# Kernel tuning notes

Measured on AMD Instinct MI355X. Metric: run time of the kernel, lower is better.

Reference implementation:

```python
import jax, jax.numpy as jnp
import numpy as np

MIN_NORM = 1e-15
PROJ_EPS = 4e-3  # float32 boundary eps used by hgcn PoincareBall.proj
C = 1.0          # curvature for every layer
N, E, D = 10000, 320000, 256


def _norm(x):
    return jnp.maximum(jnp.linalg.norm(x, axis=-1, keepdims=True), MIN_NORM)


def artanh(x):
    return jnp.arctanh(jnp.clip(x, -1 + 1e-7, 1 - 1e-7))


def proj(x, c):
    norm = _norm(x)
    maxnorm = (1.0 - PROJ_EPS) / jnp.sqrt(c)
    return jnp.where(norm > maxnorm, x / norm * maxnorm, x)


def expmap0(u, c):
    sqrt_c = jnp.sqrt(c)
    u_norm = _norm(u)
    return jnp.tanh(sqrt_c * u_norm) * u / (sqrt_c * u_norm)


def logmap0(p, c):
    sqrt_c = jnp.sqrt(c)
    p_norm = _norm(p)
    return artanh(sqrt_c * p_norm) * p / (sqrt_c * p_norm)


def mobius_add(x, y, c):
    x2 = jnp.sum(x * x, -1, keepdims=True)
    y2 = jnp.sum(y * y, -1, keepdims=True)
    xy = jnp.sum(x * y, -1, keepdims=True)
    num = (1 + 2 * c * xy + c * y2) * x + (1 - c * x2) * y
    denom = 1 + 2 * c * xy + c * c * x2 * y2
    return num / jnp.maximum(denom, MIN_NORM)


def mobius_matvec(m, x, c):
    sqrt_c = jnp.sqrt(c)
    x_norm = _norm(x)
    mx = x @ m.T
    mx_norm = _norm(mx)
    res = jnp.tanh(mx_norm / x_norm * artanh(sqrt_c * x_norm)) * mx / (mx_norm * sqrt_c)
    zero_row = jnp.all(mx == 0, axis=-1, keepdims=True)
    return jnp.where(zero_row, jnp.zeros_like(res), res)


def hgc_layer(h, W, b, edge_weight, edge_src, edge_dst, c):
    # HypLinear (dropout=0, eval mode)
    res = proj(mobius_matvec(W, h, c), c)
    hyp_bias = proj(expmap0(b[None, :], c), c)
    h = proj(mobius_add(res, hyp_bias, c), c)
    # HypAgg: tangent-space neighborhood aggregation (spmm over edge list)
    xt = logmap0(h, c)                                  # [N, D]
    msgs = edge_weight[:, None] * xt[edge_src]          # [E, D] irregular gather
    agg = jax.ops.segment_sum(msgs, edge_dst, num_segments=N)
    h = proj(expmap0(agg, c), c)
    # HypAct: relu in tangent space, map back with c_out
    xt = jax.nn.relu(logmap0(h, c))
    return proj(expmap0(xt, c), c)


def setup_inputs() -> dict:
    key = jax.random.key(0)
    ks = jax.random.split(key, 8)
    x = jax.random.normal(ks[0], (N, D), dtype=jnp.float32)
    edge_src = jax.random.randint(ks[1], (E,), 0, N)
    edge_dst = jax.random.randint(ks[2], (E,), 0, N)
    # normalized-adjacency-like positive weights (~1/deg scale)
    edge_weight = jax.random.uniform(ks[3], (E,), dtype=jnp.float32) / 32.0
    s = 1.0 / np.sqrt(D)
    W1 = jax.random.normal(ks[4], (D, D), dtype=jnp.float32) * s
    b1 = jnp.zeros((D,), dtype=jnp.float32)
    W2 = jax.random.normal(ks[5], (D, D), dtype=jnp.float32) * s
    b2 = jnp.zeros((D,), dtype=jnp.float32)
    return {"x": x, "W1": W1, "b1": b1, "W2": W2, "b2": b2,
            "edge_weight": edge_weight, "edge_src": edge_src, "edge_dst": edge_dst}


def reference(x, W1, b1, W2, b2, edge_weight, edge_src, edge_dst):
    # old=True path: map Euclidean features onto the Poincare ball first
    h = proj(expmap0(x, C), C)
    h = hgc_layer(h, W1, b1, edge_weight, edge_src, edge_dst, C)
    h = hgc_layer(h, W2, b2, edge_weight, edge_src, edge_dst, C)
    return h
```

## Files before the change

### kernel.cpp

```cpp
#include <hip/hip_runtime.h>
#include <hip/hip_fp16.h>

#define DIM 256
#define MAXNORM 0.996f
#define MINN 1e-15f
#define CLIPV 0.9999999f
#define CAP 128

typedef __attribute__((ext_vector_type(8))) short bf16x8;
typedef __attribute__((ext_vector_type(4))) float f32x4;

__device__ __forceinline__ unsigned short f2bf(float f) {
    unsigned int u = __float_as_uint(f);
    u += 0x7fffu + ((u >> 16) & 1u);
    return (unsigned short)(u >> 16);
}
__device__ __forceinline__ float h2f(unsigned short h) {
    return __half2float(__ushort_as_half(h));
}
__device__ __forceinline__ unsigned short f2h(float f) {
    return __half_as_ushort(__float2half(f));
}
__device__ __forceinline__ float wsum(float v) {
    v += __shfl_xor(v, 32);
    v += __shfl_xor(v, 16);
    v += __shfl_xor(v, 8);
    v += __shfl_xor(v, 4);
    v += __shfl_xor(v, 2);
    v += __shfl_xor(v, 1);
    return v;
}
__device__ __forceinline__ float gsum16(float v) {
    v += __shfl_xor(v, 8);
    v += __shfl_xor(v, 4);
    v += __shfl_xor(v, 2);
    v += __shfl_xor(v, 1);
    return v;
}

__global__ void k_setup(const float* __restrict__ x, unsigned short* __restrict__ h_bf,
                        float* __restrict__ hnorm2, int nrows,
                        int* __restrict__ cnt,
                        const float* __restrict__ W1, const float* __restrict__ W2,
                        unsigned short* __restrict__ w_bf, int nPerW, int eB) {
    int bid = blockIdx.x;
    if (bid < eB) {
        int gid = bid * 256 + threadIdx.x;
        int row = gid >> 6, lane = gid & 63;
        if (row >= nrows) return;
        size_t base = (size_t)row * DIM + lane * 4;
        float4 v = *(const float4*)(x + base);
        float ss = wsum(v.x * v.x + v.y * v.y + v.z * v.z + v.w * v.w);
        float n = fmaxf(sqrtf(ss), MINN);
        float tn = tanhf(n);
        float hn = (tn > MAXNORM) ? MAXNORM : tn;
        float s = hn / n;
        ushort4 ob;
        ob.x = f2bf(v.x * s); ob.y = f2bf(v.y * s);
        ob.z = f2bf(v.z * s); ob.w = f2bf(v.w * s);
        *(ushort4*)(h_bf + base) = ob;
        if (lane == 0) hnorm2[row] = hn * hn;
    } else if (bid < eB + 8) {
        int i = (bid - eB) * 256 + threadIdx.x;
        int stride = 8 * 256;
        for (; i < nrows; i += stride) cnt[i] = 0;
    } else {
        int i = (bid - eB - 8) * 256 + threadIdx.x;
        int stride = 128 * 256;
        for (; i < 2 * nPerW; i += stride)
            w_bf[i] = f2bf(i < nPerW ? W1[i] : W2[i - nPerW]);
    }
}

__global__ void k_fill(const int* __restrict__ esrc, const int* __restrict__ edst,
                       const float* __restrict__ ew, int* __restrict__ cnt,
                       int2* __restrict__ bucket, int nE, int nrows) {
    int e = blockIdx.x * blockDim.x + threadIdx.x;
    if (e >= nE) return;
    int d = edst[e];
    if (d < 0 || d >= nrows) return;
    int pos = atomicAdd(&cnt[d], 1);
    if (pos < CAP)
        bucket[(size_t)d * CAP + pos] = make_int2(esrc[e], __float_as_int(ew[e]));
}

__global__ void k_gemm_post(const unsigned short* __restrict__ Abf,
                            const unsigned short* __restrict__ Wbf,
                            const float* __restrict__ hnorm2,
                            const float* __restrict__ bias,
                            unsigned short* __restrict__ XT, int M) {
    int wave = threadIdx.x >> 6;
    int lane = threadIdx.x & 63;
    int r = lane & 15, oct = lane >> 4;
    int i0 = (blockIdx.x * 4 + wave) * 16;
    int arow = i0 + r;
    bool av = arow < M;
    const unsigned short* ap = Abf + (size_t)(av ? arow : 0) * DIM + oct * 8;
    const unsigned short* wp = Wbf + (size_t)r * DIM + oct * 8;
    const bf16x8 zf = {0, 0, 0, 0, 0, 0, 0, 0};
    f32x4 acc[16];
#pragma unroll
    for (int jt = 0; jt < 16; ++jt) acc[jt] = (f32x4){0.f, 0.f, 0.f, 0.f};
    for (int k0 = 0; k0 < 256; k0 += 32) {
        bf16x8 a = av ? *(const bf16x8*)(ap + k0) : zf;
#pragma unroll
        for (int jt = 0; jt < 16; ++jt) {
            bf16x8 w = *(const bf16x8*)(wp + (size_t)jt * 16 * DIM + k0);
            acc[jt] = __builtin_amdgcn_mfma_f32_16x16x32_bf16(a, w, acc[jt], 0, 0, 0);
        }
    }
    float bv[16];
    float bss = 0.f;
#pragma unroll
    for (int jt = 0; jt < 16; ++jt) {
        bv[jt] = bias[jt * 16 + r];
        bss = fmaf(bv[jt], bv[jt], bss);
    }
    bss = gsum16(bss);
    float bn = fmaxf(sqrtf(bss), MINN);
    float btn = tanhf(bn);
    float bhn = (btn > MAXNORM) ? MAXNORM : btn;
    float bscale = bhn / bn;
    float y2 = bhn * bhn;
#pragma unroll
    for (int jt = 0; jt < 16; ++jt) bv[jt] *= bscale;

#pragma unroll
    for (int q = 0; q < 4; ++q) {
        int row = i0 + oct * 4 + q;
        float sm = 0.f, sxy = 0.f;
#pragma unroll
        for (int jt = 0; jt < 16; ++jt) {
            float m = acc[jt][q];
            sm  = fmaf(m, m, sm);
            sxy = fmaf(m, bv[jt], sxy);
        }
        sm = gsum16(sm);
        sxy = gsum16(sxy);
        if (row < M) {
            float sh = hnorm2[row];
            float xn = fmaxf(sqrtf(sh), MINN);
            float at = atanhf(fminf(xn, CLIPV));
            float mn = fmaxf(sqrtf(sm), MINN);
            float t = tanhf(mn / xn * at);
            float alpha = t / mn;
            float resn = t;
            if (t > MAXNORM) { alpha = MAXNORM / mn; resn = MAXNORM; }
            float x2 = resn * resn;
            float xy = alpha * sxy;
            float Aa = 1.f + 2.f * xy + y2;
            float Bb = 1.f - x2;
            float den = fmaxf(1.f + 2.f * xy + x2 * y2, MINN);
            float s_m = Aa * alpha / den;
            float s_b = Bb / den;
            float hn2 = (Aa * Aa * x2 + 2.f * Aa * Bb * xy + Bb * Bb * y2) / (den * den);
            float hn = fmaxf(sqrtf(fmaxf(hn2, 0.f)), MINN);
            if (hn > MAXNORM) { float f = MAXNORM / hn; s_m *= f; s_b *= f; hn = MAXNORM; }
            float lt = atanhf(fminf(hn, CLIPV)) / hn;
            s_m *= lt; s_b *= lt;
#pragma unroll
            for (int jt = 0; jt < 16; ++jt)
                XT[(size_t)row * DIM + jt * 16 + r] = f2h(fmaf(s_m, acc[jt][q], s_b * bv[jt]));
        }
    }
}

__global__ void k_agg_finish(const unsigned short* __restrict__ XT, const int* __restrict__ cnt,
                             const int2* __restrict__ bucket,
                             float* __restrict__ OUT, unsigned short* __restrict__ OUT_bf,
                             float* __restrict__ hnorm2, int nrows) {
    int gid = blockIdx.x * blockDim.x + threadIdx.x;
    int row = gid >> 6, lane = gid & 63;
    if (row >= nrows) return;
    int deg = cnt[row];
    if (deg > CAP) deg = CAP;
    const int2* cpk = bucket + (size_t)row * CAP;
    int p1 = deg;
    float a0 = 0.f, a1 = 0.f, a2 = 0.f, a3 = 0.f;
    int p = 0;
    for (; p + 7 < p1; p += 8) {
        ushort4 v[8];
        float w[8];
#pragma unroll
        for (int u = 0; u < 8; ++u) {
            int2 pk = cpk[p + u];
            w[u] = __int_as_float(pk.y);
            v[u] = *(const ushort4*)(XT + (size_t)pk.x * DIM + lane * 4);
        }
#pragma unroll
        for (int u = 0; u < 8; ++u) {
            a0 = fmaf(w[u], h2f(v[u].x), a0);
            a1 = fmaf(w[u], h2f(v[u].y), a1);
            a2 = fmaf(w[u], h2f(v[u].z), a2);
            a3 = fmaf(w[u], h2f(v[u].w), a3);
        }
    }
    for (; p < p1; ++p) {
        int2 pk = cpk[p];
        float w = __int_as_float(pk.y);
        ushort4 v = *(const ushort4*)(XT + (size_t)pk.x * DIM + lane * 4);
        a0 = fmaf(w, h2f(v.x), a0); a1 = fmaf(w, h2f(v.y), a1);
        a2 = fmaf(w, h2f(v.z), a2); a3 = fmaf(w, h2f(v.w), a3);
    }
    float ss = wsum(a0 * a0 + a1 * a1 + a2 * a2 + a3 * a3);
    float n = fmaxf(sqrtf(ss), MINN);
    float tn = tanhf(n);
    float hn = (tn > MAXNORM) ? MAXNORM : tn;
    float s1 = hn / n;
    float lt = atanhf(fminf(hn, CLIPV)) / fmaxf(hn, MINN);
    float s2 = lt * s1;
    float x0 = fmaxf(s2 * a0, 0.f), x1 = fmaxf(s2 * a1, 0.f);
    float x2 = fmaxf(s2 * a2, 0.f), x3 = fmaxf(s2 * a3, 0.f);
    float ss2 = wsum(x0 * x0 + x1 * x1 + x2 * x2 + x3 * x3);
    float n2 = fmaxf(sqrtf(ss2), MINN);
    float tn2 = tanhf(n2);
    float hn2c = (tn2 > MAXNORM) ? MAXNORM : tn2;
    float s3 = hn2c / n2;
    float o0 = s3 * x0, o1 = s3 * x1, o2 = s3 * x2, o3 = s3 * x3;
    size_t base = (size_t)row * DIM + lane * 4;
    if (OUT_bf) {
        ushort4 ob;
        ob.x = f2bf(o0); ob.y = f2bf(o1); ob.z = f2bf(o2); ob.w = f2bf(o3);
        *(ushort4*)(OUT_bf + base) = ob;
        if (lane == 0) hnorm2[row] = hn2c * hn2c;
    } else {
        *(float4*)(OUT + base) = make_float4(o0, o1, o2, o3);
    }
}

static inline size_t align256(size_t x) { return (x + 255) & ~(size_t)255; }

extern "C" void kernel_launch(void* const* d_in, const int* in_sizes, int n_in,
                              void* d_out, int out_size, void* d_ws, size_t ws_size,
                              hipStream_t stream) {
    const float* x  = (const float*)d_in[0];
    const float* W1 = (const float*)d_in[1];
    const float* b1 = (const float*)d_in[2];
    const float* W2 = (const float*)d_in[3];
    const float* b2 = (const float*)d_in[4];
    const float* ew = (const float*)d_in[5];
    const int* esrc = (const int*)d_in[6];
    const int* edst = (const int*)d_in[7];
    const int nE = in_sizes[5];
    const int M  = in_sizes[0] / DIM;

    size_t S = (size_t)M * DIM;
    char* base = (char*)d_ws;
    size_t o = 0;
    int2* bucket   = (int2*)(base + o);          o = align256(o + (size_t)M * CAP * 8);
    int* cnt       = (int*)(base + o);           o = align256(o + (size_t)M * 4);
    float* hnorm2  = (float*)(base + o);         o = align256(o + (size_t)(M + 64) * 4);
    unsigned short* xt   = (unsigned short*)(base + o);  o = align256(o + S * 2);
    unsigned short* h_bf = (unsigned short*)(base + o);  o = align256(o + S * 2);
    unsigned short* w_bf = (unsigned short*)(base + o);  o = align256(o + (size_t)2 * DIM * DIM * 2);

    int rowBlocks = (M + 3) / 4;
    int edgeBlocks = (nE + 255) / 256;

    k_setup<<<rowBlocks + 8 + 128, 256, 0, stream>>>(
        x, h_bf, hnorm2, M, cnt, W1, W2, w_bf, DIM * DIM, rowBlocks);

    k_fill<<<edgeBlocks, 256, 0, stream>>>(esrc, edst, ew, cnt, bucket, nE, M);

    for (int layer = 0; layer < 2; ++layer) {
        const float* b = (layer == 0) ? b1 : b2;
        const unsigned short* Wb = w_bf + (size_t)layer * DIM * DIM;
        k_gemm_post<<<(M + 63) / 64, 256, 0, stream>>>(h_bf, Wb, hnorm2, b, xt, M);
        k_agg_finish<<<rowBlocks, 256, 0, stream>>>(
            xt, cnt, bucket,
            (layer == 0) ? (float*)nullptr : (float*)d_out,
            (layer == 0) ? h_bf : (unsigned short*)nullptr,
            hnorm2, M);
    }
}
```

Measured before the change: 199.9 us.

## Fuse layer-1 aggregation with layer-2 GEMM and post-processing in one kernel

Replaces the layer-1 aggregation kernel and the layer-2 GEMM/post kernel with a single kernel. Each block aggregates 16 rows into LDS as bf16, then runs MFMA against W2 and applies the mobius/logmap epilogue, writing the layer-2 tangent features. This removes the round trip of h_bf and hnorm2 through global memory and one launch. In exchange, each block uses only 16 rows, so W2 is re-read from global/L2 per block, the GEMM tile is small, and per-row work has to cross LDS with extra syncs.

```diff
diff --git a/kernel.cpp b/kernel.cpp
--- a/kernel.cpp
+++ b/kernel.cpp
@@ -6,6 +6,7 @@
 #define MINN 1e-15f
 #define CLIPV 0.9999999f
 #define CAP 128
+#define LDW 264
 
 typedef __attribute__((ext_vector_type(8))) short bf16x8;
 typedef __attribute__((ext_vector_type(4))) float f32x4;
@@ -165,20 +166,169 @@
     }
 }
 
+__global__ void __launch_bounds__(256) k_fused(
+                        const unsigned short* __restrict__ XT,
+                        const int* __restrict__ cnt, const int2* __restrict__ bucket,
+                        const unsigned short* __restrict__ Wbf,
+                        const float* __restrict__ bias,
+                        unsigned short* __restrict__ XT2, int M) {
+    __shared__ unsigned short ldsA[16][LDW];
+    __shared__ float lds_hn2[16];
+    __shared__ float lds_sm[4][16];
+    __shared__ float lds_sxy[4][16];
+    int wave = threadIdx.x >> 6;
+    int lane = threadIdx.x & 63;
+    int i0 = blockIdx.x * 16;
+
+    for (int i = 0; i < 4; ++i) {
+        int row16 = wave * 4 + i;
+        int row = i0 + row16;
+        if (row >= M) continue;
+        int deg = cnt[row];
+        if (deg > CAP) deg = CAP;
+        const int2* cpk = bucket + (size_t)row * CAP;
+        float a0 = 0.f, a1 = 0.f, a2 = 0.f, a3 = 0.f;
+        int p = 0;
+        for (; p + 7 < deg; p += 8) {
+            ushort4 v[8];
+            float w[8];
+#pragma unroll
+            for (int u = 0; u < 8; ++u) {
+                int2 pk = cpk[p + u];
+                w[u] = __int_as_float(pk.y);
+                v[u] = *(const ushort4*)(XT + (size_t)pk.x * DIM + lane * 4);
+            }
+#pragma unroll
+            for (int u = 0; u < 8; ++u) {
+                a0 = fmaf(w[u], h2f(v[u].x), a0);
+                a1 = fmaf(w[u], h2f(v[u].y), a1);
+                a2 = fmaf(w[u], h2f(v[u].z), a2);
+                a3 = fmaf(w[u], h2f(v[u].w), a3);
+            }
+        }
+        for (; p < deg; ++p) {
+            int2 pk = cpk[p];
+            float w = __int_as_float(pk.y);
+            ushort4 v = *(const ushort4*)(XT + (size_t)pk.x * DIM + lane * 4);
+            a0 = fmaf(w, h2f(v.x), a0); a1 = fmaf(w, h2f(v.y), a1);
+            a2 = fmaf(w, h2f(v.z), a2); a3 = fmaf(w, h2f(v.w), a3);
+        }
+        float ss = wsum(a0 * a0 + a1 * a1 + a2 * a2 + a3 * a3);
+        float n = fmaxf(sqrtf(ss), MINN);
+        float tn = tanhf(n);
+        float hn = (tn > MAXNORM) ? MAXNORM : tn;
+        float s1 = hn / n;
+        float lt = atanhf(fminf(hn, CLIPV)) / fmaxf(hn, MINN);
+        float s2 = lt * s1;
+        float x0 = fmaxf(s2 * a0, 0.f), x1 = fmaxf(s2 * a1, 0.f);
+        float x2 = fmaxf(s2 * a2, 0.f), x3 = fmaxf(s2 * a3, 0.f);
+        float ss2 = wsum(x0 * x0 + x1 * x1 + x2 * x2 + x3 * x3);
+        float n2 = fmaxf(sqrtf(ss2), MINN);
+        float tn2 = tanhf(n2);
+        float hn2c = (tn2 > MAXNORM) ? MAXNORM : tn2;
+        float s3 = hn2c / n2;
+        ushort4 ob;
+        ob.x = f2bf(s3 * x0); ob.y = f2bf(s3 * x1);
+        ob.z = f2bf(s3 * x2); ob.w = f2bf(s3 * x3);
+        *(ushort4*)&ldsA[row16][lane * 4] = ob;
+        if (lane == 0) lds_hn2[row16] = hn2c * hn2c;
+    }
+    __syncthreads();
+
+    int r = lane & 15, oct = lane >> 4;
+    int jtbase = wave * 4;
+    const unsigned short* wp = Wbf + (size_t)(jtbase * 16 + r) * DIM + oct * 8;
+    f32x4 acc[4];
+#pragma unroll
+    for (int j = 0; j < 4; ++j) acc[j] = (f32x4){0.f, 0.f, 0.f, 0.f};
+#pragma unroll
+    for (int k0 = 0; k0 < 256; k0 += 32) {
+        bf16x8 a = *(const bf16x8*)&ldsA[r][oct * 8 + k0];
+#pragma unroll
+        for (int j = 0; j < 4; ++j) {
+            bf16x8 w = *(const bf16x8*)(wp + (size_t)j * 16 * DIM + k0);
+            acc[j] = __builtin_amdgcn_mfma_f32_16x16x32_bf16(a, w, acc[j], 0, 0, 0);
+        }
+    }
+    float bss = 0.f;
+#pragma unroll
+    for (int jt = 0; jt < 16; ++jt) {
+        float b = bias[jt * 16 + r];
+        bss = fmaf(b, b, bss);
+    }
+    bss = gsum16(bss);
+    float bn = fmaxf(sqrtf(bss), MINN);
+    float btn = tanhf(bn);
+    float bhn = (btn > MAXNORM) ? MAXNORM : btn;
+    float bscale = bhn / bn;
+    float y2 = bhn * bhn;
+    float bvw[4];
+#pragma unroll
+    for (int j = 0; j < 4; ++j) bvw[j] = bias[(jtbase + j) * 16 + r] * bscale;
+#pragma unroll
+    for (int q = 0; q < 4; ++q) {
+        float sm = 0.f, sxy = 0.f;
+#pragma unroll
+        for (int j = 0; j < 4; ++j) {
+            float m = acc[j][q];
+            sm  = fmaf(m, m, sm);
+            sxy = fmaf(m, bvw[j], sxy);
+        }
+        sm = gsum16(sm);
+        sxy = gsum16(sxy);
+        if (r == 0) {
+            lds_sm[wave][oct * 4 + q] = sm;
+            lds_sxy[wave][oct * 4 + q] = sxy;
+        }
+    }
+    __syncthreads();
+#pragma unroll
+    for (int q = 0; q < 4; ++q) {
+        int row16 = oct * 4 + q;
+        int row = i0 + row16;
+        float sm  = lds_sm[0][row16] + lds_sm[1][row16] + lds_sm[2][row16] + lds_sm[3][row16];
+        float sxy = lds_sxy[0][row16] + lds_sxy[1][row16] + lds_sxy[2][row16] + lds_sxy[3][row16];
+        if (row < M) {
+            float sh = lds_hn2[row16];
+            float xn = fmaxf(sqrtf(sh), MINN);
+            float at = atanhf(fminf(xn, CLIPV));
+            float mn = fmaxf(sqrtf(sm), MINN);
+            float t = tanhf(mn / xn * at);
+            float alpha = t / mn;
+            float resn = t;
+            if (t > MAXNORM) { alpha = MAXNORM / mn; resn = MAXNORM; }
+            float x2 = resn * resn;
+            float xy = alpha * sxy;
+            float Aa = 1.f + 2.f * xy + y2;
+            float Bb = 1.f - x2;
+            float den = fmaxf(1.f + 2.f * xy + x2 * y2, MINN);
+            float s_m = Aa * alpha / den;
+            float s_b = Bb / den;
+            float hn2 = (Aa * Aa * x2 + 2.f * Aa * Bb * xy + Bb * Bb * y2) / (den * den);
+            float hn = fmaxf(sqrtf(fmaxf(hn2, 0.f)), MINN);
+            if (hn > MAXNORM) { float f = MAXNORM / hn; s_m *= f; s_b *= f; hn = MAXNORM; }
+            float lt = atanhf(fminf(hn, CLIPV)) / hn;
+            s_m *= lt; s_b *= lt;
+#pragma unroll
+            for (int j = 0; j < 4; ++j)
+                XT2[(size_t)row * DIM + (jtbase + j) * 16 + r] =
+                    f2h(fmaf(s_m, acc[j][q], s_b * bvw[j]));
+        }
+    }
+}
+
 __global__ void k_agg_finish(const unsigned short* __restrict__ XT, const int* __restrict__ cnt,
                              const int2* __restrict__ bucket,
-                             float* __restrict__ OUT, unsigned short* __restrict__ OUT_bf,
-                             float* __restrict__ hnorm2, int nrows) {
+                             float* __restrict__ OUT, int nrows) {
     int gid = blockIdx.x * blockDim.x + threadIdx.x;
     int row = gid >> 6, lane = gid & 63;
     if (row >= nrows) return;
     int deg = cnt[row];
     if (deg > CAP) deg = CAP;
     const int2* cpk = bucket + (size_t)row * CAP;
-    int p1 = deg;
     float a0 = 0.f, a1 = 0.f, a2 = 0.f, a3 = 0.f;
     int p = 0;
-    for (; p + 7 < p1; p += 8) {
+    for (; p + 7 < deg; p += 8) {
         ushort4 v[8];
         float w[8];
 #pragma unroll
@@ -195,7 +345,7 @@
             a3 = fmaf(w[u], h2f(v[u].w), a3);
         }
     }
-    for (; p < p1; ++p) {
+    for (; p < deg; ++p) {
         int2 pk = cpk[p];
         float w = __int_as_float(pk.y);
         ushort4 v = *(const ushort4*)(XT + (size_t)pk.x * DIM + lane * 4);
@@ -216,16 +366,8 @@
     float tn2 = tanhf(n2);
     float hn2c = (tn2 > MAXNORM) ? MAXNORM : tn2;
     float s3 = hn2c / n2;
-    float o0 = s3 * x0, o1 = s3 * x1, o2 = s3 * x2, o3 = s3 * x3;
     size_t base = (size_t)row * DIM + lane * 4;
-    if (OUT_bf) {
-        ushort4 ob;
-        ob.x = f2bf(o0); ob.y = f2bf(o1); ob.z = f2bf(o2); ob.w = f2bf(o3);
-        *(ushort4*)(OUT_bf + base) = ob;
-        if (lane == 0) hnorm2[row] = hn2c * hn2c;
-    } else {
-        *(float4*)(OUT + base) = make_float4(o0, o1, o2, o3);
-    }
+    *(float4*)(OUT + base) = make_float4(s3 * x0, s3 * x1, s3 * x2, s3 * x3);
 }
 
 static inline size_t align256(size_t x) { return (x + 255) & ~(size_t)255; }
@@ -251,6 +393,7 @@
     int* cnt       = (int*)(base + o);           o = align256(o + (size_t)M * 4);
     float* hnorm2  = (float*)(base + o);         o = align256(o + (size_t)(M + 64) * 4);
     unsigned short* xt   = (unsigned short*)(base + o);  o = align256(o + S * 2);
+    unsigned short* xt2  = (unsigned short*)(base + o);  o = align256(o + S * 2);
     unsigned short* h_bf = (unsigned short*)(base + o);  o = align256(o + S * 2);
     unsigned short* w_bf = (unsigned short*)(base + o);  o = align256(o + (size_t)2 * DIM * DIM * 2);
 
@@ -259,17 +402,9 @@
 
     k_setup<<<rowBlocks + 8 + 128, 256, 0, stream>>>(
         x, h_bf, hnorm2, M, cnt, W1, W2, w_bf, DIM * DIM, rowBlocks);
-
     k_fill<<<edgeBlocks, 256, 0, stream>>>(esrc, edst, ew, cnt, bucket, nE, M);
-
-    for (int layer = 0; layer < 2; ++layer) {
-        const float* b = (layer == 0) ? b1 : b2;
-        const unsigned short* Wb = w_bf + (size_t)layer * DIM * DIM;
-        k_gemm_post<<<(M + 63) / 64, 256, 0, stream>>>(h_bf, Wb, hnorm2, b, xt, M);
-        k_agg_finish<<<rowBlocks, 256, 0, stream>>>(
-            xt, cnt, bucket,
-            (layer == 0) ? (float*)nullptr : (float*)d_out,
-            (layer == 0) ? h_bf : (unsigned short*)nullptr,
-            hnorm2, M);
-    }
-}
+    k_gemm_post<<<(M + 63) / 64, 256, 0, stream>>>(h_bf, w_bf, hnorm2, b1, xt, M);
+    k_fused<<<(M + 15) / 16, 256, 0, stream>>>(
+        xt, cnt, bucket, w_bf + (size_t)DIM * DIM, b2, xt2, M);
+    k_agg_finish<<<rowBlocks, 256, 0, stream>>>(xt2, cnt, bucket, (float*)d_out, M);
+}
```

After: 200.8 us. About the same (+0.4%).

## Split aggregation by source-row half to improve gather cache locality

Applied to the files above, without the earlier changes.

Edges are bucketed per destination into two halves by source index, and aggregation runs as two kernels, each gathering only from one half of XT. Each pass then touches a smaller working set that may fit better in cache. The first pass writes float partial sums that the second reads back, which adds an extra kernel launch and extra memory traffic. Per-half capacity drops to 64, so a destination with more than 64 edges from one half would drop edges.

```diff
diff --git a/kernel.cpp b/kernel.cpp
--- a/kernel.cpp
+++ b/kernel.cpp
@@ -5,7 +5,7 @@
 #define MAXNORM 0.996f
 #define MINN 1e-15f
 #define CLIPV 0.9999999f
-#define CAP 128
+#define CAP2 64
 
 typedef __attribute__((ext_vector_type(8))) short bf16x8;
 typedef __attribute__((ext_vector_type(4))) float f32x4;
@@ -40,7 +40,7 @@
 
 __global__ void k_setup(const float* __restrict__ x, unsigned short* __restrict__ h_bf,
                         float* __restrict__ hnorm2, int nrows,
-                        int* __restrict__ cnt,
+                        int* __restrict__ cnt2,
                         const float* __restrict__ W1, const float* __restrict__ W2,
                         unsigned short* __restrict__ w_bf, int nPerW, int eB) {
     int bid = blockIdx.x;
@@ -63,7 +63,7 @@
     } else if (bid < eB + 8) {
         int i = (bid - eB) * 256 + threadIdx.x;
         int stride = 8 * 256;
-        for (; i < nrows; i += stride) cnt[i] = 0;
+        for (; i < 2 * nrows; i += stride) cnt2[i] = 0;
     } else {
         int i = (bid - eB - 8) * 256 + threadIdx.x;
         int stride = 128 * 256;
@@ -73,15 +73,17 @@
 }
 
 __global__ void k_fill(const int* __restrict__ esrc, const int* __restrict__ edst,
-                       const float* __restrict__ ew, int* __restrict__ cnt,
-                       int2* __restrict__ bucket, int nE, int nrows) {
+                       const float* __restrict__ ew, int* __restrict__ cnt2,
+                       int2* __restrict__ bucket2, int nE, int nrows, int halfM) {
     int e = blockIdx.x * blockDim.x + threadIdx.x;
     if (e >= nE) return;
     int d = edst[e];
     if (d < 0 || d >= nrows) return;
-    int pos = atomicAdd(&cnt[d], 1);
-    if (pos < CAP)
-        bucket[(size_t)d * CAP + pos] = make_int2(esrc[e], __float_as_int(ew[e]));
+    int s = esrc[e];
+    int half = (s >= halfM) ? 1 : 0;
+    int pos = atomicAdd(&cnt2[d * 2 + half], 1);
+    if (pos < CAP2)
+        bucket2[((size_t)d * 2 + half) * CAP2 + pos] = make_int2(s, __float_as_int(ew[e]));
 }
 
 __global__ void k_gemm_post(const unsigned short* __restrict__ Abf,
@@ -165,20 +167,18 @@
     }
 }
 
-__global__ void k_agg_finish(const unsigned short* __restrict__ XT, const int* __restrict__ cnt,
-                             const int2* __restrict__ bucket,
-                             float* __restrict__ OUT, unsigned short* __restrict__ OUT_bf,
-                             float* __restrict__ hnorm2, int nrows) {
+__global__ void k_aggA(const unsigned short* __restrict__ XT, const int* __restrict__ cnt2,
+                       const int2* __restrict__ bucket2,
+                       float* __restrict__ partial, int nrows) {
     int gid = blockIdx.x * blockDim.x + threadIdx.x;
     int row = gid >> 6, lane = gid & 63;
     if (row >= nrows) return;
-    int deg = cnt[row];
-    if (deg > CAP) deg = CAP;
-    const int2* cpk = bucket + (size_t)row * CAP;
-    int p1 = deg;
+    int deg = cnt2[row * 2];
+    if (deg > CAP2) deg = CAP2;
+    const int2* cpk = bucket2 + (size_t)row * 2 * CAP2;
     float a0 = 0.f, a1 = 0.f, a2 = 0.f, a3 = 0.f;
     int p = 0;
-    for (; p + 7 < p1; p += 8) {
+    for (; p + 7 < deg; p += 8) {
         ushort4 v[8];
         float w[8];
 #pragma unroll
@@ -195,13 +195,55 @@
             a3 = fmaf(w[u], h2f(v[u].w), a3);
         }
     }
-    for (; p < p1; ++p) {
+    for (; p < deg; ++p) {
         int2 pk = cpk[p];
         float w = __int_as_float(pk.y);
         ushort4 v = *(const ushort4*)(XT + (size_t)pk.x * DIM + lane * 4);
         a0 = fmaf(w, h2f(v.x), a0); a1 = fmaf(w, h2f(v.y), a1);
         a2 = fmaf(w, h2f(v.z), a2); a3 = fmaf(w, h2f(v.w), a3);
     }
+    *(float4*)(partial + (size_t)row * DIM + lane * 4) = make_float4(a0, a1, a2, a3);
+}
+
+__global__ void k_aggB(const unsigned short* __restrict__ XT, const int* __restrict__ cnt2,
+                       const int2* __restrict__ bucket2, const float* __restrict__ partial,
+                       float* __restrict__ OUT, unsigned short* __restrict__ OUT_bf,
+                       float* __restrict__ hnorm2, int nrows) {
+    int gid = blockIdx.x * blockDim.x + threadIdx.x;
+    int row = gid >> 6, lane = gid & 63;
+    if (row >= nrows) return;
+    int deg = cnt2[row * 2 + 1];
+    if (deg > CAP2) deg = CAP2;
+    const int2* cpk = bucket2 + ((size_t)row * 2 + 1) * CAP2;
+    float a0 = 0.f, a1 = 0.f, a2 = 0.f, a3 = 0.f;
+    int p = 0;
+    for (; p + 7 < deg; p += 8) {
+        ushort4 v[8];
+        float w[8];
+#pragma unroll
+        for (int u = 0; u < 8; ++u) {
+            int2 pk = cpk[p + u];
+            w[u] = __int_as_float(pk.y);
+            v[u] = *(const ushort4*)(XT + (size_t)pk.x * DIM + lane * 4);
+        }
+#pragma unroll
+        for (int u = 0; u < 8; ++u) {
+            a0 = fmaf(w[u], h2f(v[u].x), a0);
+            a1 = fmaf(w[u], h2f(v[u].y), a1);
+            a2 = fmaf(w[u], h2f(v[u].z), a2);
+            a3 = fmaf(w[u], h2f(v[u].w), a3);
+        }
+    }
+    for (; p < deg; ++p) {
+        int2 pk = cpk[p];
+        float w = __int_as_float(pk.y);
+        ushort4 v = *(const ushort4*)(XT + (size_t)pk.x * DIM + lane * 4);
+        a0 = fmaf(w, h2f(v.x), a0); a1 = fmaf(w, h2f(v.y), a1);
+        a2 = fmaf(w, h2f(v.z), a2); a3 = fmaf(w, h2f(v.w), a3);
+    }
+    float4 pp = *(const float4*)(partial + (size_t)row * DIM + lane * 4);
+    a0 += pp.x; a1 += pp.y; a2 += pp.z; a3 += pp.w;
+
     float ss = wsum(a0 * a0 + a1 * a1 + a2 * a2 + a3 * a3);
     float n = fmaxf(sqrtf(ss), MINN);
     float tn = tanhf(n);
@@ -247,8 +289,9 @@
     size_t S = (size_t)M * DIM;
     char* base = (char*)d_ws;
     size_t o = 0;
-    int2* bucket   = (int2*)(base + o);          o = align256(o + (size_t)M * CAP * 8);
-    int* cnt       = (int*)(base + o);           o = align256(o + (size_t)M * 4);
+    int2* bucket2  = (int2*)(base + o);          o = align256(o + (size_t)M * 2 * CAP2 * 8);
+    int* cnt2      = (int*)(base + o);           o = align256(o + (size_t)2 * M * 4);
+    float* partial = (float*)(base + o);         o = align256(o + S * 4);
     float* hnorm2  = (float*)(base + o);         o = align256(o + (size_t)(M + 64) * 4);
     unsigned short* xt   = (unsigned short*)(base + o);  o = align256(o + S * 2);
     unsigned short* h_bf = (unsigned short*)(base + o);  o = align256(o + S * 2);
@@ -258,16 +301,15 @@
     int edgeBlocks = (nE + 255) / 256;
 
     k_setup<<<rowBlocks + 8 + 128, 256, 0, stream>>>(
-        x, h_bf, hnorm2, M, cnt, W1, W2, w_bf, DIM * DIM, rowBlocks);
-
-    k_fill<<<edgeBlocks, 256, 0, stream>>>(esrc, edst, ew, cnt, bucket, nE, M);
-
+        x, h_bf, hnorm2, M, cnt2, W1, W2, w_bf, DIM * DIM, rowBlocks);
+    k_fill<<<edgeBlocks, 256, 0, stream>>>(esrc, edst, ew, cnt2, bucket2, nE, M, M / 2);
     for (int layer = 0; layer < 2; ++layer) {
         const float* b = (layer == 0) ? b1 : b2;
         const unsigned short* Wb = w_bf + (size_t)layer * DIM * DIM;
         k_gemm_post<<<(M + 63) / 64, 256, 0, stream>>>(h_bf, Wb, hnorm2, b, xt, M);
-        k_agg_finish<<<rowBlocks, 256, 0, stream>>>(
-            xt, cnt, bucket,
+        k_aggA<<<rowBlocks, 256, 0, stream>>>(xt, cnt2, bucket2, partial, M);
+        k_aggB<<<rowBlocks, 256, 0, stream>>>(
+            xt, cnt2, bucket2, partial,
             (layer == 0) ? (float*)nullptr : (float*)d_out,
             (layer == 0) ? h_bf : (unsigned short*)nullptr,
             hnorm2, M);
```

After: 205.4 us. +2.7%, slower.
